# Kernel tuning notes

Hardware: AMD Instinct MI355X
Metric: run time of the kernel (lower is better)

## Reference

```python
import jax, jax.numpy as jnp
import numpy as np

BILATERAL = True
THETA_ALPHA = 8.0   # spatial bandwidth for bilateral term
THETA_BETA = 0.5    # color bandwidth for bilateral term
THETA_GAMMA = 3.0   # spatial bandwidth for spatial-only term


def _features(input_image):
    # input_image: [B, Ci, H, W] -> features [B, N, D]
    B, Ci, H, W = input_image.shape
    N = H * W
    ys, xs = jnp.meshgrid(jnp.arange(H, dtype=jnp.float32),
                          jnp.arange(W, dtype=jnp.float32), indexing='ij')
    pos = jnp.stack([ys, xs], axis=-1).reshape(N, 2)  # [N, 2]
    if BILATERAL:
        sp = jnp.broadcast_to(pos / THETA_ALPHA, (B, N, 2))
        col = input_image.reshape(B, Ci, N).transpose(0, 2, 1) / THETA_BETA  # [B, N, Ci]
        return jnp.concatenate([sp, col], axis=-1)  # [B, N, 2+Ci]
    else:
        return jnp.broadcast_to(pos / THETA_GAMMA, (B, N, 2))


def _gauss_filter(values, feats):
    # values: [B, C, N]; feats: [B, N, D] -> [B, C, N]
    # K_ij = exp(-0.5 * ||f_i - f_j||^2) (unnormalized, as in permutohedral filtering)
    sq = jnp.sum(feats * feats, axis=-1)  # [B, N]
    # squared distances: [B, N, N]
    d2 = sq[:, :, None] + sq[:, None, :] - 2.0 * jnp.einsum('bnd,bmd->bnm', feats, feats)
    K = jnp.exp(-0.5 * jnp.maximum(d2, 0.0))
    return jnp.einsum('bnm,bcm->bcn', K, values)


def setup_inputs() -> dict:
    key = jax.random.key(0)
    k1, k2 = jax.random.split(key)
    cur_state = jax.random.normal(k1, (2, 21, 96, 96), dtype=jnp.float32)
    input_image = jax.random.uniform(k2, (2, 3, 96, 96), dtype=jnp.float32)
    return {"cur_state": cur_state, "input_image": input_image}


def reference(cur_state, input_image):
    assert cur_state.ndim == 4
    B, C, H, W = cur_state.shape
    N = H * W
    feats = _features(input_image)                 # [B, N, D]
    vals = cur_state.reshape(B, C, N)              # [B, C, N]
    out = _gauss_filter(vals, feats)               # [B, C, N]
    return out.reshape(B, C, H, W)
```

## Files before the change

### kernel.cpp

```cpp
#include <hip/hip_runtime.h>
#include <hip/hip_bf16.h>
#include <math.h>


#define HH 96
#define WW 96
#define NN (HH * WW)
#define NB 2
#define NC 21

typedef __attribute__((ext_vector_type(8))) short short8;
typedef __attribute__((ext_vector_type(16))) float f32x16;

constexpr float INV_TA = 0.125f;
constexpr float INV_TB = 2.0f;
constexpr float LOG2E  = 1.44269504088896340736f;

constexpr int BLK    = 256;
constexpr int ITILE  = 64;
constexpr int NIT    = NN / ITILE;
constexpr int G      = 12;
constexpr int JG     = NN / G;
constexpr int JS     = 256;
constexpr int NP     = JG / JS;
constexpr int NPIECE = NN / JS;
constexpr int NJB    = JS / 32;

constexpr size_t VG_BYTES  = (size_t)NB * NPIECE * 1024 * 16;
constexpr size_t FJA_OFF   = VG_BYTES;
constexpr int VLDS_BYTES   = 1024 * 16;
constexpr int FJA_LDS_OFF  = VLDS_BYTES;
constexpr int SMEM_BYTES   = VLDS_BYTES + 2 * 256 * 16;

constexpr int NVU  = NB * NPIECE * 1024;
constexpr int NFT  = NB * NN;
constexpr int PREP_TASKS = NVU + NFT;

#if defined(__has_builtin)
#if __has_builtin(__builtin_amdgcn_exp2f)
#define EXP2F(x) __builtin_amdgcn_exp2f(x)
#endif
#endif
#ifndef EXP2F
#define EXP2F(x) exp2f(x)
#endif

__device__ __forceinline__ unsigned short bf16_rne(float f) {
    __hip_bfloat16 h = __float2bfloat16(f);
    unsigned short u; __builtin_memcpy(&u, &h, 2); return u;
}
__device__ __forceinline__ float bf16_f(unsigned short u) {
    __hip_bfloat16 h; __builtin_memcpy(&h, &u, 2); return __bfloat162float(h);
}
__device__ __forceinline__ unsigned pk2(float a, float b) {
    const unsigned u0 = __float_as_uint(a) + 0x8000u;
    const unsigned u1 = __float_as_uint(b) + 0x8000u;
    return __builtin_amdgcn_perm(u1, u0, 0x07060302u);
}

__global__ __launch_bounds__(BLK)
void prep_kernel(const float* __restrict__ cur, const float* __restrict__ img,
                 unsigned char* __restrict__ ws) {
    const int t = blockIdx.x * BLK + threadIdx.x;
    if (t < NVU) {
        const int b  = t / (NPIECE * 1024);
        const int r  = t % (NPIECE * 1024);
        const int rr = r & 1023;
        const int piece = r >> 10;
        const int jbl = rr >> 7;
        const int m   = (rr >> 6) & 1;
        const int h   = (rr >> 5) & 1;
        const int c   = rr & 31;
        const int jb = piece * 256 + jbl * 32 + m * 16 + 4 * h;
        float4 qa = {0, 0, 0, 0}, qb = {0, 0, 0, 0};
        if (c < NC) {
            const float* row = cur + ((size_t)b * NC + c) * NN;
            qa = *(const float4*)(row + jb);
            qb = *(const float4*)(row + jb + 8);
        }
        uint4 o;
        o.x = pk2(qa.x, qa.y); o.y = pk2(qa.z, qa.w);
        o.z = pk2(qb.x, qb.y); o.w = pk2(qb.z, qb.w);
        *(uint4*)(ws + (size_t)t * 16) = o;
    } else {
        const int tf = t - NVU;
        const int b = tf / NN;
        const int j = tf % NN;
        const float y = (float)(j / WW) * INV_TA;
        const float x = (float)(j % WW) * INV_TA;
        const float* ib = img + (size_t)b * 3 * NN;
        unsigned short ch[3], cl[3]; float cf[3];
        #pragma unroll
        for (int d = 0; d < 3; ++d) {
            const float c = ib[d * NN + j] * INV_TB;
            ch[d] = bf16_rne(c);
            const float chf = bf16_f(ch[d]);
            cl[d] = bf16_rne(c - chf);
            cf[d] = chf + bf16_f(cl[d]);
        }
        const float e = -0.5f * (y * y + x * x +
                                 cf[0] * cf[0] + cf[1] * cf[1] + cf[2] * cf[2]);
        const unsigned short eh = bf16_rne(e);
        const unsigned short el = bf16_rne(e - bf16_f(eh));
        const unsigned short yb = bf16_rne(y), xb = bf16_rne(x);
        const unsigned short one = 0x3F80;
        const int piece = j >> 8, jl = j & 255;
        unsigned short* u0 = (unsigned short*)
            (ws + FJA_OFF + ((((size_t)b * NPIECE + piece) * 2 + 0) * 256 + jl) * 16);
        unsigned short* u1 = (unsigned short*)
            (ws + FJA_OFF + ((((size_t)b * NPIECE + piece) * 2 + 1) * 256 + jl) * 16);
        u0[0] = yb; u0[1] = xb; u0[2] = ch[0]; u0[3] = ch[1]; u0[4] = ch[2];
        u0[5] = cl[0]; u0[6] = cl[1]; u0[7] = cl[2];
        u1[0] = ch[0]; u1[1] = ch[1]; u1[2] = ch[2]; u1[3] = eh; u1[4] = el;
        u1[5] = one; u1[6] = one; u1[7] = 0;
    }
}

__global__ __launch_bounds__(BLK)
void perm_gauss_mfma(const float* __restrict__ img,
                     const unsigned char* __restrict__ ws,
                     float* __restrict__ out) {
    __shared__ __align__(16) unsigned char smem[SMEM_BYTES];
    const int tid  = threadIdx.x;
    const int lane = tid & 63;
    const int wave = tid >> 6;
    const int isub = wave & 1;
    const int jh   = wave >> 1;
    const int il   = lane & 31;
    const int half = lane >> 5;

    const int it = blockIdx.x, g = blockIdx.y, b = blockIdx.z;
    const int ibase = it * ITILE;
    const float* imgb = img + (size_t)b * 3 * NN;
    float* outb = out + (size_t)b * NC * NN;

    const int ig = ibase + isub * 32 + il;
    const float y = (float)(ig / WW) * INV_TA;
    const float x = (float)(ig % WW) * INV_TA;
    unsigned short ch[3], cl[3]; float cf[3];
    #pragma unroll
    for (int d = 0; d < 3; ++d) {
        const float c = imgb[d * NN + ig] * INV_TB;
        ch[d] = bf16_rne(c);
        const float chf = bf16_f(ch[d]);
        cl[d] = bf16_rne(c - chf);
        cf[d] = chf + bf16_f(cl[d]);
    }
    const float e = -0.5f * (y * y + x * x +
                             cf[0] * cf[0] + cf[1] * cf[1] + cf[2] * cf[2]);
    const unsigned short eh = bf16_rne(e);
    const unsigned short el = bf16_rne(e - bf16_f(eh));
    const unsigned short one = 0x3F80;
    union { unsigned short u[8]; short8 v; } bfi;
    if (half == 0) {
        bfi.u[0] = bf16_rne(y); bfi.u[1] = bf16_rne(x);
        bfi.u[2] = ch[0]; bfi.u[3] = ch[1]; bfi.u[4] = ch[2];
        bfi.u[5] = ch[0]; bfi.u[6] = ch[1]; bfi.u[7] = ch[2];
    } else {
        bfi.u[0] = cl[0]; bfi.u[1] = cl[1]; bfi.u[2] = cl[2];
        bfi.u[3] = one; bfi.u[4] = one; bfi.u[5] = eh; bfi.u[6] = el;
        bfi.u[7] = 0;
    }

    f32x16 acc, zz;
    #pragma unroll
    for (int r = 0; r < 16; ++r) { acc[r] = 0.0f; zz[r] = 0.0f; }

    for (int p = 0; p < NP; ++p) {
        const int pidx = g * NP + p;
        __syncthreads();
        const float4* vsrc = (const float4*)(ws + ((size_t)b * NPIECE + pidx) * 16384);
        float4* vdst = (float4*)smem;
        #pragma unroll
        for (int k = 0; k < 4; ++k) vdst[k * 256 + tid] = vsrc[k * 256 + tid];
        const float4* fsrc = (const float4*)
            (ws + FJA_OFF + ((size_t)b * NPIECE + pidx) * 8192);
        float4* fdst = (float4*)(smem + FJA_LDS_OFF);
        #pragma unroll
        for (int k = 0; k < 2; ++k) fdst[k * 256 + tid] = fsrc[k * 256 + tid];
        __syncthreads();

        #pragma unroll
        for (int q = 0; q < 4; ++q) {
            const int jbl = jh * 4 + q;
            const short8 afj = *(const short8*)
                (smem + FJA_LDS_OFF + (size_t)(half * 256 + jbl * 32 + il) * 16);
            const f32x16 s =
                __builtin_amdgcn_mfma_f32_32x32x16_bf16(afj, bfi.v, zz, 0, 0, 0);
            float w[16];
            #pragma unroll
            for (int r = 0; r < 16; ++r) w[r] = EXP2F(s[r] * LOG2E);
            union { unsigned dw[4]; short8 v; } a1, a2;
            #pragma unroll
            for (int d = 0; d < 4; ++d) {
                a1.dw[d] = pk2(w[2 * d],     w[2 * d + 1]);
                a2.dw[d] = pk2(w[8 + 2 * d], w[9 + 2 * d]);
            }
            const short8 v1 = *(const short8*)
                (smem + (size_t)((4 * jbl + half) * 32 + il) * 16);
            const short8 v2 = *(const short8*)
                (smem + (size_t)((4 * jbl + 2 + half) * 32 + il) * 16);
            acc = __builtin_amdgcn_mfma_f32_32x32x16_bf16(a1.v, v1, acc, 0, 0, 0);
            acc = __builtin_amdgcn_mfma_f32_32x32x16_bf16(a2.v, v2, acc, 0, 0, 0);
        }
    }

    __syncthreads();
    float* mytile = (float*)smem + wave * 32 * 33;
    #pragma unroll
    for (int r = 0; r < 16; ++r) {
        const int row = (r & 3) + 8 * (r >> 2) + 4 * half;
        mytile[row * 33 + il] = acc[r];
    }
    #pragma unroll
    for (int cc = 0; cc < 11; ++cc) {
        const int c = 2 * cc + half;
        if (c < NC) {
            const float v = mytile[il * 33 + c];
            atomicAdd(&outb[(size_t)c * NN + ibase + isub * 32 + il], v);
        }
    }
}

extern "C" void kernel_launch(void* const* d_in, const int* in_sizes, int n_in,
                              void* d_out, int out_size, void* d_ws, size_t ws_size,
                              hipStream_t stream) {
    const float* cur = (const float*)d_in[0];
    const float* img = (const float*)d_in[1];
    float* out = (float*)d_out;
    unsigned char* ws = (unsigned char*)d_ws;

    hipMemsetAsync(out, 0, (size_t)NB * NC * NN * sizeof(float), stream);
    prep_kernel<<<PREP_TASKS / BLK, BLK, 0, stream>>>(cur, img, ws);
    dim3 grid(NIT, G, NB);
    perm_gauss_mfma<<<grid, BLK, 0, stream>>>(img, ws, out);
}
```

Before: 97.10 us.

## Load j-tile operands directly from global with register prefetch, drop LDS staging

Each wave now owns its own 32-row i-tile (ITILE becomes 128, G becomes 8) and streams the feature and value fragments for its j-range straight from global memory into registers, prefetching the next step's fragments one iteration ahead. This removes the cooperative LDS staging and the two __syncthreads per piece. The prep kernel's workspace layout is simplified to match, with per-column feature rows and per-32-block value fragments. In exchange there is no reuse of j data across waves inside a block, so L2/global traffic rises, and there are fewer blocks in the grid.

```diff
diff --git a/kernel.cpp b/kernel.cpp
--- a/kernel.cpp
+++ b/kernel.cpp
@@ -16,24 +16,18 @@
 constexpr float INV_TB = 2.0f;
 constexpr float LOG2E  = 1.44269504088896340736f;
 
-constexpr int BLK    = 256;
-constexpr int ITILE  = 64;
-constexpr int NIT    = NN / ITILE;
-constexpr int G      = 12;
-constexpr int JG     = NN / G;
-constexpr int JS     = 256;
-constexpr int NP     = JG / JS;
-constexpr int NPIECE = NN / JS;
-constexpr int NJB    = JS / 32;
-
-constexpr size_t VG_BYTES  = (size_t)NB * NPIECE * 1024 * 16;
-constexpr size_t FJA_OFF   = VG_BYTES;
-constexpr int VLDS_BYTES   = 1024 * 16;
-constexpr int FJA_LDS_OFF  = VLDS_BYTES;
-constexpr int SMEM_BYTES   = VLDS_BYTES + 2 * 256 * 16;
-
-constexpr int NVU  = NB * NPIECE * 1024;
-constexpr int NFT  = NB * NN;
+constexpr int BLK   = 256;
+constexpr int ITILE = 128;
+constexpr int NIT   = NN / ITILE;
+constexpr int NJB   = NN / 32;
+constexpr int G     = 8;
+constexpr int QW    = NJB / G;
+
+constexpr size_t VG_BYTES = (size_t)NB * NJB * 128 * 16;
+constexpr size_t FJA_OFF  = VG_BYTES;
+
+constexpr int NVU = NB * NJB * 128;
+constexpr int NFT = NB * NN;
 constexpr int PREP_TASKS = NVU + NFT;
 
 #if defined(__has_builtin)
@@ -63,15 +57,13 @@
                  unsigned char* __restrict__ ws) {
     const int t = blockIdx.x * BLK + threadIdx.x;
     if (t < NVU) {
-        const int b  = t / (NPIECE * 1024);
-        const int r  = t % (NPIECE * 1024);
-        const int rr = r & 1023;
-        const int piece = r >> 10;
-        const int jbl = rr >> 7;
-        const int m   = (rr >> 6) & 1;
-        const int h   = (rr >> 5) & 1;
-        const int c   = rr & 31;
-        const int jb = piece * 256 + jbl * 32 + m * 16 + 4 * h;
+        const int c    = t & 31;
+        const int h    = (t >> 5) & 1;
+        const int m    = (t >> 6) & 1;
+        const int jw   = t >> 7;
+        const int b    = jw / NJB;
+        const int jblk = jw % NJB;
+        const int jb = jblk * 32 + m * 16 + 4 * h;
         float4 qa = {0, 0, 0, 0}, qb = {0, 0, 0, 0};
         if (c < NC) {
             const float* row = cur + ((size_t)b * NC + c) * NN;
@@ -104,11 +96,10 @@
         const unsigned short el = bf16_rne(e - bf16_f(eh));
         const unsigned short yb = bf16_rne(y), xb = bf16_rne(x);
         const unsigned short one = 0x3F80;
-        const int piece = j >> 8, jl = j & 255;
         unsigned short* u0 = (unsigned short*)
-            (ws + FJA_OFF + ((((size_t)b * NPIECE + piece) * 2 + 0) * 256 + jl) * 16);
+            (ws + FJA_OFF + ((size_t)(b * 2 + 0) * NN + j) * 16);
         unsigned short* u1 = (unsigned short*)
-            (ws + FJA_OFF + ((((size_t)b * NPIECE + piece) * 2 + 1) * 256 + jl) * 16);
+            (ws + FJA_OFF + ((size_t)(b * 2 + 1) * NN + j) * 16);
         u0[0] = yb; u0[1] = xb; u0[2] = ch[0]; u0[3] = ch[1]; u0[4] = ch[2];
         u0[5] = cl[0]; u0[6] = cl[1]; u0[7] = cl[2];
         u1[0] = ch[0]; u1[1] = ch[1]; u1[2] = ch[2]; u1[3] = eh; u1[4] = el;
@@ -120,21 +111,19 @@
 void perm_gauss_mfma(const float* __restrict__ img,
                      const unsigned char* __restrict__ ws,
                      float* __restrict__ out) {
-    __shared__ __align__(16) unsigned char smem[SMEM_BYTES];
+    __shared__ __align__(16) float tile[4 * 32 * 33];
     const int tid  = threadIdx.x;
     const int lane = tid & 63;
     const int wave = tid >> 6;
-    const int isub = wave & 1;
-    const int jh   = wave >> 1;
     const int il   = lane & 31;
     const int half = lane >> 5;
 
     const int it = blockIdx.x, g = blockIdx.y, b = blockIdx.z;
-    const int ibase = it * ITILE;
+    const int ibase = it * ITILE + wave * 32;
     const float* imgb = img + (size_t)b * 3 * NN;
     float* outb = out + (size_t)b * NC * NN;
 
-    const int ig = ibase + isub * 32 + il;
+    const int ig = ibase + il;
     const float y = (float)(ig / WW) * INV_TA;
     const float x = (float)(ig % WW) * INV_TA;
     unsigned short ch[3], cl[3]; float cf[3];
@@ -166,47 +155,44 @@
     #pragma unroll
     for (int r = 0; r < 16; ++r) { acc[r] = 0.0f; zz[r] = 0.0f; }
 
-    for (int p = 0; p < NP; ++p) {
-        const int pidx = g * NP + p;
-        __syncthreads();
-        const float4* vsrc = (const float4*)(ws + ((size_t)b * NPIECE + pidx) * 16384);
-        float4* vdst = (float4*)smem;
+    const int jb0 = g * QW;
+    const unsigned char* fp = ws + FJA_OFF +
+        ((size_t)(b * 2 + half) * NN + (size_t)jb0 * 32 + il) * 16;
+    const unsigned char* vp = ws +
+        ((size_t)(b * NJB + jb0) * 128 + half * 32 + il) * 16;
+
+    short8 af = *(const short8*)fp;
+    short8 v1 = *(const short8*)vp;
+    short8 v2 = *(const short8*)(vp + 1024);
+
+    auto qstep = [&](short8 A, short8 V1, short8 V2) {
+        const f32x16 s =
+            __builtin_amdgcn_mfma_f32_32x32x16_bf16(A, bfi.v, zz, 0, 0, 0);
+        float w[16];
         #pragma unroll
-        for (int k = 0; k < 4; ++k) vdst[k * 256 + tid] = vsrc[k * 256 + tid];
-        const float4* fsrc = (const float4*)
-            (ws + FJA_OFF + ((size_t)b * NPIECE + pidx) * 8192);
-        float4* fdst = (float4*)(smem + FJA_LDS_OFF);
+        for (int r = 0; r < 16; ++r) w[r] = EXP2F(s[r] * LOG2E);
+        union { unsigned dw[4]; short8 v; } a1, a2;
         #pragma unroll
-        for (int k = 0; k < 2; ++k) fdst[k * 256 + tid] = fsrc[k * 256 + tid];
-        __syncthreads();
-
-        #pragma unroll
-        for (int q = 0; q < 4; ++q) {
-            const int jbl = jh * 4 + q;
-            const short8 afj = *(const short8*)
-                (smem + FJA_LDS_OFF + (size_t)(half * 256 + jbl * 32 + il) * 16);
-            const f32x16 s =
-                __builtin_amdgcn_mfma_f32_32x32x16_bf16(afj, bfi.v, zz, 0, 0, 0);
-            float w[16];
-            #pragma unroll
-            for (int r = 0; r < 16; ++r) w[r] = EXP2F(s[r] * LOG2E);
-            union { unsigned dw[4]; short8 v; } a1, a2;
-            #pragma unroll
-            for (int d = 0; d < 4; ++d) {
-                a1.dw[d] = pk2(w[2 * d],     w[2 * d + 1]);
-                a2.dw[d] = pk2(w[8 + 2 * d], w[9 + 2 * d]);
-            }
-            const short8 v1 = *(const short8*)
-                (smem + (size_t)((4 * jbl + half) * 32 + il) * 16);
-            const short8 v2 = *(const short8*)
-                (smem + (size_t)((4 * jbl + 2 + half) * 32 + il) * 16);
-            acc = __builtin_amdgcn_mfma_f32_32x32x16_bf16(a1.v, v1, acc, 0, 0, 0);
-            acc = __builtin_amdgcn_mfma_f32_32x32x16_bf16(a2.v, v2, acc, 0, 0, 0);
-        }
-    }
-
-    __syncthreads();
-    float* mytile = (float*)smem + wave * 32 * 33;
+        for (int d = 0; d < 4; ++d) {
+            a1.dw[d] = pk2(w[2 * d],     w[2 * d + 1]);
+            a2.dw[d] = pk2(w[8 + 2 * d], w[9 + 2 * d]);
+        }
+        acc = __builtin_amdgcn_mfma_f32_32x32x16_bf16(a1.v, V1, acc, 0, 0, 0);
+        acc = __builtin_amdgcn_mfma_f32_32x32x16_bf16(a2.v, V2, acc, 0, 0, 0);
+    };
+
+    #pragma unroll 2
+    for (int q = 0; q < QW - 1; ++q) {
+        fp += 512; vp += 2048;
+        const short8 afn = *(const short8*)fp;
+        const short8 v1n = *(const short8*)vp;
+        const short8 v2n = *(const short8*)(vp + 1024);
+        qstep(af, v1, v2);
+        af = afn; v1 = v1n; v2 = v2n;
+    }
+    qstep(af, v1, v2);
+
+    float* mytile = tile + wave * (32 * 33);
     #pragma unroll
     for (int r = 0; r < 16; ++r) {
         const int row = (r & 3) + 8 * (r >> 2) + 4 * half;
@@ -217,7 +203,7 @@
         const int c = 2 * cc + half;
         if (c < NC) {
             const float v = mytile[il * 33 + c];
-            atomicAdd(&outb[(size_t)c * NN + ibase + isub * 32 + il], v);
+            atomicAdd(&outb[(size_t)c * NN + ibase + il], v);
         }
     }
 }
```

Result: faster. 94.50 us (-2.7%).
